# Performance work log

Hardware: AMD Instinct MI355X
Metric: run time of the kernel (lower is better)

Reference implementation:

```python
import jax, jax.numpy as jnp
import numpy as np

N_FEATURES = 26          # number of feature categories (FEATURE_AND_ENCODER entries)
VOCAB_PER_FEATURE = 50000  # ids in [f*V, (f+1)*V) belong to feature f
SLOTS_PER_FEATURE = 8
BATCH = 16384
EMBED = 32
VOCAB = N_FEATURES * VOCAB_PER_FEATURE


def setup_inputs() -> dict:
    key = jax.random.key(0)
    ks = jax.random.split(key, 8)
    P = N_FEATURES * SLOTS_PER_FEATURE  # 208 ids per row
    x = jax.random.randint(ks[0], (BATCH, P), 0, VOCAB, dtype=jnp.int64)
    table = jax.random.normal(ks[1], (VOCAB, EMBED), dtype=jnp.float32) * 0.1
    D = N_FEATURES * EMBED  # 832
    W0 = jax.random.normal(ks[2], (D, 64), dtype=jnp.float32) * (1.0 / np.sqrt(D))
    b0 = jax.random.normal(ks[3], (64,), dtype=jnp.float32) * 0.01
    W1 = jax.random.normal(ks[4], (64, 16), dtype=jnp.float32) * (1.0 / 8.0)
    b1 = jax.random.normal(ks[5], (16,), dtype=jnp.float32) * 0.01
    W2 = jax.random.normal(ks[6], (16, 1), dtype=jnp.float32) * 0.25
    return {"x": x, "table": table, "W0": W0, "b0": b0, "W1": W1, "b1": b1, "W2": W2}


def reference(x, table, W0, b0, W1, b1, W2):
    B = x.shape[0]
    # dynamic embedding lookup: [B, P, E]
    embeds = table[x]
    # category of each id (what encoder.match_category encodes): [B, P]
    cat = x // VOCAB_PER_FEATURE
    # mask+gather+reduce_sum per feature == one-hot segment sum over features
    onehot = jax.nn.one_hot(cat, N_FEATURES, dtype=table.dtype)  # [B, P, F]
    pooled = jnp.einsum('bpe,bpf->bfe', embeds, onehot)          # [B, F, E]
    feats = pooled.reshape(B, N_FEATURES * EMBED)                # concat of per-feature sums
    h = jax.nn.relu(feats @ W0 + b0)
    h = jax.nn.relu(h @ W1 + b1)
    logits = h @ W2
    return jax.nn.sigmoid(logits)
```

## Files before the change

kernel.cpp:

```cpp
#include <hip/hip_runtime.h>
#include <math.h>

#define BATCH 16384
#define PP    208
#define NF    26
#define VPF   50000u
#define EMB   32
#define DD    832

__global__ __launch_bounds__(256) void pool_kernel(const int* __restrict__ x,
                                                   const float* __restrict__ table,
                                                   float* __restrict__ feats) {
    __shared__ int   s_ids[8 * PP];
    __shared__ float s_pool[8 * DD];

    const int tid  = threadIdx.x;
    const int row0 = blockIdx.x * 8;

    for (int i = tid; i < 8 * DD; i += 256) s_pool[i] = 0.0f;
    for (int i = tid; i < 8 * PP; i += 256) s_ids[i] = x[(size_t)row0 * PP + i];
    __syncthreads();

    const int wave = tid >> 6;
    const int lane = tid & 63;
    const int sub  = lane >> 5;
    const int e    = lane & 31;
    const int r    = wave * 2 + sub;

    float*     pool = s_pool + r * DD + e;
    const int* ids  = s_ids + r * PP;

#pragma unroll 4
    for (int p = 0; p < PP; ++p) {
        const unsigned id  = (unsigned)ids[p];
        const unsigned cat = id / VPF;
        const float    v   = table[(size_t)id * EMB + e];
        atomicAdd(pool + cat * EMB, v);
    }
    __syncthreads();

    for (int i = tid; i < 8 * DD; i += 256)
        feats[(size_t)row0 * DD + i] = s_pool[i];
}

#define TM 64
#define BK 64

__global__ __launch_bounds__(256) void mlp_kernel(const float* __restrict__ feats,
                                                  const float* __restrict__ W0,
                                                  const float* __restrict__ b0,
                                                  const float* __restrict__ W1,
                                                  const float* __restrict__ b1,
                                                  const float* __restrict__ W2,
                                                  float* __restrict__ out) {
    __shared__ float sF[TM][BK + 1];
    __shared__ float sW[BK][64];
    __shared__ float sH[TM][64 + 1];
    __shared__ float sW1[64 * 16];
    __shared__ float sB0[64];
    __shared__ float sB1[16];
    __shared__ float sW2[16];

    const int tid  = threadIdx.x;
    const int row0 = blockIdx.x * TM;

    for (int i = tid; i < 64 * 16; i += 256) sW1[i] = W1[i];
    if (tid < 64) sB0[tid] = b0[tid];
    if (tid < 16) sB1[tid] = b1[tid];
    if (tid < 16) sW2[tid] = W2[tid];

    const int tcol = tid & 15;
    const int trow = tid >> 4;

    float acc[4][4];
#pragma unroll
    for (int i = 0; i < 4; ++i)
#pragma unroll
        for (int j = 0; j < 4; ++j) acc[i][j] = 0.0f;

    for (int kt = 0; kt < DD; kt += BK) {
        __syncthreads();
        for (int i = tid; i < TM * BK; i += 256) {
            const int rr = i >> 6, kk = i & 63;
            sF[rr][kk] = feats[(size_t)(row0 + rr) * DD + kt + kk];
        }
        for (int i = tid; i < BK * 64; i += 256) {
            const int kk = i >> 6, cc = i & 63;
            sW[kk][cc] = W0[(size_t)(kt + kk) * 64 + cc];
        }
        __syncthreads();

#pragma unroll
        for (int k = 0; k < BK; ++k) {
            const float4 wv = *reinterpret_cast<const float4*>(&sW[k][tcol << 2]);
            float f[4];
#pragma unroll
            for (int i = 0; i < 4; ++i) f[i] = sF[trow * 4 + i][k];
#pragma unroll
            for (int i = 0; i < 4; ++i) {
                acc[i][0] = fmaf(f[i], wv.x, acc[i][0]);
                acc[i][1] = fmaf(f[i], wv.y, acc[i][1]);
                acc[i][2] = fmaf(f[i], wv.z, acc[i][2]);
                acc[i][3] = fmaf(f[i], wv.w, acc[i][3]);
            }
        }
    }

    __syncthreads();
#pragma unroll
    for (int i = 0; i < 4; ++i)
#pragma unroll
        for (int j = 0; j < 4; ++j) {
            const int c = (tcol << 2) + j;
            sH[trow * 4 + i][c] = fmaxf(acc[i][j] + sB0[c], 0.0f);
        }
    __syncthreads();

    if (tid < TM) {
        float h1[16];
#pragma unroll
        for (int j = 0; j < 16; ++j) h1[j] = sB1[j];
        for (int k = 0; k < 64; ++k) {
            const float h = sH[tid][k];
#pragma unroll
            for (int j = 0; j < 16; ++j)
                h1[j] = fmaf(h, sW1[k * 16 + j], h1[j]);
        }
        float z = 0.0f;
#pragma unroll
        for (int j = 0; j < 16; ++j)
            z = fmaf(fmaxf(h1[j], 0.0f), sW2[j], z);
        out[row0 + tid] = 1.0f / (1.0f + expf(-z));
    }
}

extern "C" void kernel_launch(void* const* d_in, const int* in_sizes, int n_in,
                              void* d_out, int out_size, void* d_ws, size_t ws_size,
                              hipStream_t stream) {
    const int*   x     = (const int*)d_in[0];
    const float* table = (const float*)d_in[1];
    const float* W0    = (const float*)d_in[2];
    const float* b0    = (const float*)d_in[3];
    const float* W1    = (const float*)d_in[4];
    const float* b1    = (const float*)d_in[5];
    const float* W2    = (const float*)d_in[6];
    float*       out   = (float*)d_out;

    float* feats = (float*)d_ws;

    pool_kernel<<<BATCH / 8, 256, 0, stream>>>(x, table, feats);
    mlp_kernel<<<BATCH / TM, 256, 0, stream>>>(feats, W0, b0, W1, b1, W2, out);
}
```

Baseline: 813.0 us.

## Use bf16 MFMA for first MLP layer and restructure pooling per row

```diff
diff --git a/kernel.cpp b/kernel.cpp
--- a/kernel.cpp
+++ b/kernel.cpp
@@ -8,129 +8,147 @@
 #define EMB   32
 #define DD    832
 
-__global__ __launch_bounds__(256) void pool_kernel(const int* __restrict__ x,
-                                                   const float* __restrict__ table,
-                                                   float* __restrict__ feats) {
-    __shared__ int   s_ids[8 * PP];
-    __shared__ float s_pool[8 * DD];
+typedef __attribute__((ext_vector_type(8))) short short8v;
+typedef __attribute__((ext_vector_type(4))) float float4v;
 
-    const int tid  = threadIdx.x;
-    const int row0 = blockIdx.x * 8;
+static __device__ __forceinline__ ushort f32_to_bf16(float f) {
+    unsigned u = __builtin_bit_cast(unsigned, f);
+    unsigned r = (u + 0x7fffu + ((u >> 16) & 1u)) >> 16;
+    return (ushort)r;
+}
 
-    for (int i = tid; i < 8 * DD; i += 256) s_pool[i] = 0.0f;
-    for (int i = tid; i < 8 * PP; i += 256) s_ids[i] = x[(size_t)row0 * PP + i];
+__global__ __launch_bounds__(256) void prep_kernel(const float* __restrict__ W0,
+                                                   ushort* __restrict__ w0p) {
+    const int i = blockIdx.x * 256 + threadIdx.x;
+    if (i < DD * 64) {
+        const int k = i >> 6, c = i & 63;
+        const int kt = k >> 5, kk = k & 31;
+        w0p[(kt * 64 + c) * 32 + kk] = f32_to_bf16(W0[i]);
+    }
+}
+
+__global__ __launch_bounds__(256, 8) void pool_kernel(const int* __restrict__ x,
+                                                      const float* __restrict__ table,
+                                                      ushort* __restrict__ feats) {
+    __shared__ int   s_ids[PP];
+    __shared__ float s_pool[DD];
+
+    const int    tid = threadIdx.x;
+    const size_t row = blockIdx.x;
+
+    for (int i = tid; i < DD; i += 256) s_pool[i] = 0.0f;
+    if (tid < PP) s_ids[tid] = x[row * PP + tid];
     __syncthreads();
 
-    const int wave = tid >> 6;
-    const int lane = tid & 63;
-    const int sub  = lane >> 5;
-    const int e    = lane & 31;
-    const int r    = wave * 2 + sub;
+    const int e  = tid & 31;
+    const int p0 = (tid >> 5) * 26;
+    float* pool  = s_pool + e;
 
-    float*     pool = s_pool + r * DD + e;
-    const int* ids  = s_ids + r * PP;
-
-#pragma unroll 4
-    for (int p = 0; p < PP; ++p) {
-        const unsigned id  = (unsigned)ids[p];
-        const unsigned cat = id / VPF;
-        const float    v   = table[(size_t)id * EMB + e];
-        atomicAdd(pool + cat * EMB, v);
+#pragma unroll 1
+    for (int b = 0; b < 24; b += 4) {
+        const unsigned id0 = (unsigned)s_ids[p0 + b + 0];
+        const unsigned id1 = (unsigned)s_ids[p0 + b + 1];
+        const unsigned id2 = (unsigned)s_ids[p0 + b + 2];
+        const unsigned id3 = (unsigned)s_ids[p0 + b + 3];
+        const float v0 = table[(size_t)id0 * EMB + e];
+        const float v1 = table[(size_t)id1 * EMB + e];
+        const float v2 = table[(size_t)id2 * EMB + e];
+        const float v3 = table[(size_t)id3 * EMB + e];
+        atomicAdd(pool + (id0 / VPF) * EMB, v0);
+        atomicAdd(pool + (id1 / VPF) * EMB, v1);
+        atomicAdd(pool + (id2 / VPF) * EMB, v2);
+        atomicAdd(pool + (id3 / VPF) * EMB, v3);
+    }
+    {
+        const unsigned idA = (unsigned)s_ids[p0 + 24];
+        const unsigned idB = (unsigned)s_ids[p0 + 25];
+        const float vA = table[(size_t)idA * EMB + e];
+        const float vB = table[(size_t)idB * EMB + e];
+        atomicAdd(pool + (idA / VPF) * EMB, vA);
+        atomicAdd(pool + (idB / VPF) * EMB, vB);
     }
     __syncthreads();
 
-    for (int i = tid; i < 8 * DD; i += 256)
-        feats[(size_t)row0 * DD + i] = s_pool[i];
+    if (tid < DD / 4) {
+        ushort4 o;
+        o.x = f32_to_bf16(s_pool[tid * 4 + 0]);
+        o.y = f32_to_bf16(s_pool[tid * 4 + 1]);
+        o.z = f32_to_bf16(s_pool[tid * 4 + 2]);
+        o.w = f32_to_bf16(s_pool[tid * 4 + 3]);
+        *reinterpret_cast<ushort4*>(feats + row * DD + tid * 4) = o;
+    }
 }
 
-#define TM 64
-#define BK 64
-
-__global__ __launch_bounds__(256) void mlp_kernel(const float* __restrict__ feats,
-                                                  const float* __restrict__ W0,
+__global__ __launch_bounds__(256) void mlp_kernel(const ushort* __restrict__ feats,
+                                                  const ushort* __restrict__ w0p,
                                                   const float* __restrict__ b0,
                                                   const float* __restrict__ W1,
                                                   const float* __restrict__ b1,
                                                   const float* __restrict__ W2,
                                                   float* __restrict__ out) {
-    __shared__ float sF[TM][BK + 1];
-    __shared__ float sW[BK][64];
-    __shared__ float sH[TM][64 + 1];
-    __shared__ float sW1[64 * 16];
-    __shared__ float sB0[64];
-    __shared__ float sB1[16];
-    __shared__ float sW2[16];
+    __shared__ float sH[64][65];
+    __shared__ float sH1[64][17];
 
-    const int tid  = threadIdx.x;
-    const int row0 = blockIdx.x * TM;
+    const int tid   = threadIdx.x;
+    const int wave  = tid >> 6;
+    const int lane  = tid & 63;
+    const int lrow  = lane & 15;
+    const int lk    = lane >> 4;
+    const int brow0 = blockIdx.x * 64;
 
-    for (int i = tid; i < 64 * 16; i += 256) sW1[i] = W1[i];
-    if (tid < 64) sB0[tid] = b0[tid];
-    if (tid < 16) sB1[tid] = b1[tid];
-    if (tid < 16) sW2[tid] = W2[tid];
+    float4v acc[4];
+#pragma unroll
+    for (int n = 0; n < 4; ++n) acc[n] = (float4v){0.f, 0.f, 0.f, 0.f};
 
-    const int tcol = tid & 15;
-    const int trow = tid >> 4;
+    const ushort* frow  = feats + (size_t)(brow0 + wave * 16 + lrow) * DD + lk * 8;
+    const ushort* wbase = w0p + lrow * 32 + lk * 8;
 
-    float acc[4][4];
+#pragma unroll 2
+    for (int kt = 0; kt < 26; ++kt) {
+        const short8v a = *reinterpret_cast<const short8v*>(frow + kt * 32);
 #pragma unroll
-    for (int i = 0; i < 4; ++i)
-#pragma unroll
-        for (int j = 0; j < 4; ++j) acc[i][j] = 0.0f;
-
-    for (int kt = 0; kt < DD; kt += BK) {
-        __syncthreads();
-        for (int i = tid; i < TM * BK; i += 256) {
-            const int rr = i >> 6, kk = i & 63;
-            sF[rr][kk] = feats[(size_t)(row0 + rr) * DD + kt + kk];
-        }
-        for (int i = tid; i < BK * 64; i += 256) {
-            const int kk = i >> 6, cc = i & 63;
-            sW[kk][cc] = W0[(size_t)(kt + kk) * 64 + cc];
-        }
-        __syncthreads();
-
-#pragma unroll
-        for (int k = 0; k < BK; ++k) {
-            const float4 wv = *reinterpret_cast<const float4*>(&sW[k][tcol << 2]);
-            float f[4];
-#pragma unroll
-            for (int i = 0; i < 4; ++i) f[i] = sF[trow * 4 + i][k];
-#pragma unroll
-            for (int i = 0; i < 4; ++i) {
-                acc[i][0] = fmaf(f[i], wv.x, acc[i][0]);
-                acc[i][1] = fmaf(f[i], wv.y, acc[i][1]);
-                acc[i][2] = fmaf(f[i], wv.z, acc[i][2]);
-                acc[i][3] = fmaf(f[i], wv.w, acc[i][3]);
-            }
+        for (int n = 0; n < 4; ++n) {
+            const short8v b = *reinterpret_cast<const short8v*>(wbase + (size_t)(kt * 64 + n * 16) * 32);
+            acc[n] = __builtin_amdgcn_mfma_f32_16x16x32_bf16(a, b, acc[n], 0, 0, 0);
         }
     }
 
-    __syncthreads();
 #pragma unroll
-    for (int i = 0; i < 4; ++i)
+    for (int n = 0; n < 4; ++n) {
+        const int   col = n * 16 + lrow;
+        const float bb  = b0[col];
 #pragma unroll
-        for (int j = 0; j < 4; ++j) {
-            const int c = (tcol << 2) + j;
-            sH[trow * 4 + i][c] = fmaxf(acc[i][j] + sB0[c], 0.0f);
+        for (int r = 0; r < 4; ++r) {
+            const int rr = wave * 16 + lk * 4 + r;
+            sH[rr][col] = fmaxf(acc[n][r] + bb, 0.f);
         }
+    }
     __syncthreads();
 
-    if (tid < TM) {
-        float h1[16];
+    {
+        const int r = tid >> 2, cg = (tid & 3) * 4;
+        float a0 = b1[cg + 0], a1 = b1[cg + 1], a2 = b1[cg + 2], a3 = b1[cg + 3];
+#pragma unroll 8
+        for (int k = 0; k < 64; ++k) {
+            const float  h  = sH[r][k];
+            const float4 wv = *reinterpret_cast<const float4*>(W1 + k * 16 + cg);
+            a0 = fmaf(h, wv.x, a0);
+            a1 = fmaf(h, wv.y, a1);
+            a2 = fmaf(h, wv.z, a2);
+            a3 = fmaf(h, wv.w, a3);
+        }
+        sH1[r][cg + 0] = fmaxf(a0, 0.f);
+        sH1[r][cg + 1] = fmaxf(a1, 0.f);
+        sH1[r][cg + 2] = fmaxf(a2, 0.f);
+        sH1[r][cg + 3] = fmaxf(a3, 0.f);
+    }
+    __syncthreads();
+
+    if (tid < 64) {
+        float z = 0.f;
 #pragma unroll
-        for (int j = 0; j < 16; ++j) h1[j] = sB1[j];
-        for (int k = 0; k < 64; ++k) {
-            const float h = sH[tid][k];
-#pragma unroll
-            for (int j = 0; j < 16; ++j)
-                h1[j] = fmaf(h, sW1[k * 16 + j], h1[j]);
-        }
-        float z = 0.0f;
-#pragma unroll
-        for (int j = 0; j < 16; ++j)
-            z = fmaf(fmaxf(h1[j], 0.0f), sW2[j], z);
-        out[row0 + tid] = 1.0f / (1.0f + expf(-z));
+        for (int j = 0; j < 16; ++j) z = fmaf(sH1[tid][j], W2[j], z);
+        out[brow0 + tid] = 1.f / (1.f + expf(-z));
     }
 }
 
@@ -146,8 +164,10 @@
     const float* W2    = (const float*)d_in[6];
     float*       out   = (float*)d_out;
 
-    float* feats = (float*)d_ws;
+    ushort* feats16 = (ushort*)d_ws;
+    ushort* w0p     = feats16 + (size_t)BATCH * DD;
 
-    pool_kernel<<<BATCH / 8, 256, 0, stream>>>(x, table, feats);
-    mlp_kernel<<<BATCH / TM, 256, 0, stream>>>(feats, W0, b0, W1, b1, W2, out);
+    prep_kernel<<<(DD * 64 + 255) / 256, 256, 0, stream>>>(W0, w0p);
+    pool_kernel<<<BATCH, 256, 0, stream>>>(x, table, feats16);
+    mlp_kernel<<<BATCH / 64, 256, 0, stream>>>(feats16, w0p, b0, W1, b1, W2, out);
 }
```

Result: faster. 756.1 us (-7.0%).
